# Kernel optimization log

Measured on AMD Instinct MI355X. Metric: run time of the kernel, lower is better.

The kernel has to match this reference:

```python
import jax, jax.numpy as jnp
import numpy as np

N, CX, CS, H = 2048, 768, 384, 16
D = CX // H  # 48


def _ln(t, eps=1e-5):
    mu = jnp.mean(t, axis=-1, keepdims=True)
    var = jnp.mean(jnp.square(t - mu), axis=-1, keepdims=True)
    return (t - mu) * jax.lax.rsqrt(var + eps)


def setup_inputs() -> dict:
    key = jax.random.key(0)
    ks = jax.random.split(key, 16)
    s = 0.02
    return {
        "x": jax.random.normal(ks[0], (N, CX), jnp.float32),
        "mask": jax.random.randint(ks[1], (N,), 0, 2, jnp.int32),
        "pair_logits": jax.random.normal(ks[2], (H, N, N), jnp.float32),
        "single_cond": jax.random.normal(ks[3], (N, CS), jnp.float32),
        # AdaptiveLayerNorm params (single_cond LN has weight, no bias)
        "ln_sc_w": jnp.ones((CS,), jnp.float32),
        "sc_scale_w": s * jax.random.normal(ks[4], (CS, CX), jnp.float32),
        "sc_scale_b": jnp.zeros((CX,), jnp.float32),
        "sc_bias_w": s * jax.random.normal(ks[5], (CS, CX), jnp.float32),
        # q/k/v/gating projections (stored as (in, out); y = x @ W)
        "q_w": s * jax.random.normal(ks[6], (CX, CX), jnp.float32),
        "q_b": jnp.zeros((CX,), jnp.float32),
        "k_w": s * jax.random.normal(ks[7], (CX, CX), jnp.float32),
        "v_w": s * jax.random.normal(ks[8], (CX, CX), jnp.float32),
        "gate_w": s * jax.random.normal(ks[9], (CX, CX), jnp.float32),
        # AdaLNZero params
        "out_w": s * jax.random.normal(ks[10], (CX, CX), jnp.float32),
        "azc_w": s * jax.random.normal(ks[11], (CS, CX), jnp.float32),
        "azc_b": jnp.zeros((CX,), jnp.float32),
    }


def reference(x, mask, pair_logits, single_cond, ln_sc_w, sc_scale_w, sc_scale_b,
              sc_bias_w, q_w, q_b, k_w, v_w, gate_w, out_w, azc_w, azc_b):
    # AdaptiveLayerNorm (use_single_cond=True)
    xn = _ln(x)                              # (N, CX), no affine
    sc = _ln(single_cond) * ln_sc_w          # (N, CS), weight only
    xa = jax.nn.sigmoid(sc @ sc_scale_w + sc_scale_b) * xn + sc @ sc_bias_w

    # QKV projections, split into heads: (N, H, D)
    q = (xa @ q_w + q_b).reshape(N, H, D)
    k = (xa @ k_w).reshape(N, H, D)
    v = (xa @ v_w).reshape(N, H, D)

    # Attention with per-head additive pair bias and key mask
    logits = jnp.einsum("qhd,khd->hqk", q * (D ** -0.5), k) + pair_logits
    logits = jnp.where(mask.astype(bool)[None, None, :], logits, -1e9)
    w = jax.nn.softmax(logits, axis=-1)      # (H, N, N)
    wa = jnp.einsum("hqk,khd->qhd", w, v).reshape(N, CX)

    # Gating, then AdaLNZero output
    wa = wa * jax.nn.sigmoid(xa @ gate_w)
    out = (wa @ out_w) * jax.nn.sigmoid(sc @ azc_w + azc_b)
    return out
```

## Files before the change

kernel.cpp:

```cpp
#include <hip/hip_runtime.h>
#include <math.h>

#define NN 2048
#define CXX 768
#define CSS 384
#define HH 16
#define DHH 48

typedef short bf16x8 __attribute__((ext_vector_type(8)));
typedef float f32x4 __attribute__((ext_vector_type(4)));

#define MFMA16(a,b,c) __builtin_amdgcn_mfma_f32_16x16x32_bf16(a,b,c,0,0,0)

__device__ __forceinline__ unsigned short f2bf(float f){
  unsigned u = __float_as_uint(f);
  u += 0x7FFFu + ((u >> 16) & 1u);
  return (unsigned short)(u >> 16);
}
__device__ __forceinline__ float bf2f(unsigned short u){
  return __uint_as_float(((unsigned)u) << 16);
}
__device__ __forceinline__ void async_copy16(const void* g, void* l){
  __builtin_amdgcn_global_load_lds((const __attribute__((address_space(1))) void*)g,
                                   (__attribute__((address_space(3))) void*)l, 16, 0, 0);
}

__device__ inline float waveReduceSum(float v){
  #pragma unroll
  for(int o=32;o>0;o>>=1) v += __shfl_xor(v,o);
  return v;
}

__global__ __launch_bounds__(256) void transpose_bf16(const float* __restrict__ W,
    unsigned short* __restrict__ Wt, int K, int Ncols){
  __shared__ unsigned short t[32][33];
  int n0 = blockIdx.x*32, k0 = blockIdx.y*32;
  int c = threadIdx.x & 31, r = threadIdx.x >> 5;
  #pragma unroll
  for(int i=0;i<32;i+=8){
    float v = W[(size_t)(k0 + r + i)*Ncols + n0 + c];
    t[c][r+i] = f2bf(v);
  }
  __syncthreads();
  #pragma unroll
  for(int i=0;i<32;i+=8){
    Wt[(size_t)(n0 + r + i)*K + k0 + c] = t[r+i][c];
  }
}

__global__ __launch_bounds__(256) void ln_x_kernel(const float* __restrict__ x,
                                                   float* __restrict__ xn){
  int row = blockIdx.x;
  int t = threadIdx.x;
  const float* xr = x + (size_t)row*CXX;
  float v0 = xr[t], v1 = xr[t+256], v2 = xr[t+512];
  float s = v0+v1+v2;
  __shared__ float red[4], red2[4];
  s = waveReduceSum(s);
  if((t&63)==0) red[t>>6] = s;
  __syncthreads();
  float mu = (red[0]+red[1]+red[2]+red[3]) * (1.0f/CXX);
  float d0=v0-mu, d1=v1-mu, d2=v2-mu;
  float q = d0*d0+d1*d1+d2*d2;
  q = waveReduceSum(q);
  if((t&63)==0) red2[t>>6] = q;
  __syncthreads();
  float var = (red2[0]+red2[1]+red2[2]+red2[3]) * (1.0f/CXX);
  float r = rsqrtf(var + 1e-5f);
  float* o = xn + (size_t)row*CXX;
  o[t] = d0*r; o[t+256] = d1*r; o[t+512] = d2*r;
}

__global__ __launch_bounds__(128) void ln_sc_kernel(const float* __restrict__ scin,
                                                    const float* __restrict__ w,
                                                    unsigned short* __restrict__ sc){
  int row = blockIdx.x;
  int t = threadIdx.x;
  const float* xr = scin + (size_t)row*CSS;
  float v0 = xr[t], v1 = xr[t+128], v2 = xr[t+256];
  float s = v0+v1+v2;
  __shared__ float red[2], red2[2];
  s = waveReduceSum(s);
  if((t&63)==0) red[t>>6] = s;
  __syncthreads();
  float mu = (red[0]+red[1]) * (1.0f/CSS);
  float d0=v0-mu, d1=v1-mu, d2=v2-mu;
  float q = d0*d0+d1*d1+d2*d2;
  q = waveReduceSum(q);
  if((t&63)==0) red2[t>>6] = q;
  __syncthreads();
  float var = (red2[0]+red2[1]) * (1.0f/CSS);
  float r = rsqrtf(var + 1e-5f);
  unsigned short* o = sc + (size_t)row*CSS;
  o[t]     = f2bf(d0*r*w[t]);
  o[t+128] = f2bf(d1*r*w[t+128]);
  o[t+256] = f2bf(d2*r*w[t+256]);
}

template<int K, int NC, int MODE>
__global__ __launch_bounds__(256) void gemm_mfma(const unsigned short* __restrict__ A,
    const unsigned short* __restrict__ Bt, const float* __restrict__ bias,
    const float* __restrict__ mul, void* __restrict__ Cp){
  __shared__ unsigned short As[128*32];
  __shared__ unsigned short Bs[128*32];
  const int tid = threadIdx.x;
  const int w = tid>>6, lane = tid&63;
  const int ln15 = lane&15, hi = lane>>4;
  const int wm = w&1, wn = w>>1;
  const int m0 = blockIdx.y*128, n0 = blockIdx.x*128;
  const int lrow = lane>>2, lk = (lane&3)*8;

  f32x4 z = {0.f,0.f,0.f,0.f};
  f32x4 acc[4][4];
  #pragma unroll
  for(int i=0;i<4;i++)
    #pragma unroll
    for(int j=0;j<4;j++) acc[i][j] = z;

  for(int k0=0;k0<K;k0+=32){
    const unsigned short* ga = A + (size_t)(m0 + w*32 + lrow)*K + k0 + lk;
    const unsigned short* gb = Bt + (size_t)(n0 + w*32 + lrow)*K + k0 + lk;
    async_copy16(ga,          &As[w*1024]);
    async_copy16(ga + 16*K,   &As[w*1024 + 512]);
    async_copy16(gb,          &Bs[w*1024]);
    async_copy16(gb + 16*K,   &Bs[w*1024 + 512]);
    __syncthreads();
    bf16x8 af[4], bfr[4];
    #pragma unroll
    for(int i=0;i<4;i++) af[i]  = *(const bf16x8*)&As[(wm*64 + i*16 + ln15)*32 + hi*8];
    #pragma unroll
    for(int j=0;j<4;j++) bfr[j] = *(const bf16x8*)&Bs[(wn*64 + j*16 + ln15)*32 + hi*8];
    #pragma unroll
    for(int i=0;i<4;i++)
      #pragma unroll
      for(int j=0;j<4;j++)
        acc[i][j] = MFMA16(af[i], bfr[j], acc[i][j]);
    __syncthreads();
  }

  #pragma unroll
  for(int i=0;i<4;i++){
    #pragma unroll
    for(int j=0;j<4;j++){
      #pragma unroll
      for(int r=0;r<4;r++){
        int gm = m0 + wm*64 + i*16 + hi*4 + r;
        int gn = n0 + wn*64 + j*16 + ln15;
        float v = acc[i][j][r];
        if constexpr (MODE == 0){
          if(gn < 768) v += bias[gn];
          if(gn >= 2304) v = 1.0f/(1.0f + __expf(-v));
          ((unsigned short*)Cp)[(size_t)gm*NC + gn] = f2bf(v);
        } else if constexpr (MODE == 1){
          v = 1.0f/(1.0f + __expf(-(v + bias[gn])));
          ((float*)Cp)[(size_t)gm*NC + gn] = v;
        } else {
          ((float*)Cp)[(size_t)gm*NC + gn] = v * mul[(size_t)gm*NC + gn];
        }
      }
    }
  }
}

__global__ __launch_bounds__(256) void adaln_mfma(const unsigned short* __restrict__ A,
    const unsigned short* __restrict__ B1, const unsigned short* __restrict__ B2,
    const float* __restrict__ bs, const float* __restrict__ xn,
    unsigned short* __restrict__ xa){
  __shared__ unsigned short As[128*32];
  __shared__ unsigned short Bs1[128*32];
  __shared__ unsigned short Bs2[128*32];
  const int tid = threadIdx.x;
  const int w = tid>>6, lane = tid&63;
  const int ln15 = lane&15, hi = lane>>4;
  const int wm = w&1, wn = w>>1;
  const int m0 = blockIdx.y*128, n0 = blockIdx.x*128;
  const int lrow = lane>>2, lk = (lane&3)*8;

  f32x4 z = {0.f,0.f,0.f,0.f};
  f32x4 acc1[4][4], acc2[4][4];
  #pragma unroll
  for(int i=0;i<4;i++)
    #pragma unroll
    for(int j=0;j<4;j++){ acc1[i][j] = z; acc2[i][j] = z; }

  for(int k0=0;k0<CSS;k0+=32){
    const unsigned short* ga  = A  + (size_t)(m0 + w*32 + lrow)*CSS + k0 + lk;
    const unsigned short* gb1 = B1 + (size_t)(n0 + w*32 + lrow)*CSS + k0 + lk;
    const unsigned short* gb2 = B2 + (size_t)(n0 + w*32 + lrow)*CSS + k0 + lk;
    async_copy16(ga,            &As[w*1024]);
    async_copy16(ga  + 16*CSS,  &As[w*1024 + 512]);
    async_copy16(gb1,           &Bs1[w*1024]);
    async_copy16(gb1 + 16*CSS,  &Bs1[w*1024 + 512]);
    async_copy16(gb2,           &Bs2[w*1024]);
    async_copy16(gb2 + 16*CSS,  &Bs2[w*1024 + 512]);
    __syncthreads();
    bf16x8 af[4], b1f[4], b2f[4];
    #pragma unroll
    for(int i=0;i<4;i++) af[i]  = *(const bf16x8*)&As[(wm*64 + i*16 + ln15)*32 + hi*8];
    #pragma unroll
    for(int j=0;j<4;j++){
      b1f[j] = *(const bf16x8*)&Bs1[(wn*64 + j*16 + ln15)*32 + hi*8];
      b2f[j] = *(const bf16x8*)&Bs2[(wn*64 + j*16 + ln15)*32 + hi*8];
    }
    #pragma unroll
    for(int i=0;i<4;i++)
      #pragma unroll
      for(int j=0;j<4;j++){
        acc1[i][j] = MFMA16(af[i], b1f[j], acc1[i][j]);
        acc2[i][j] = MFMA16(af[i], b2f[j], acc2[i][j]);
      }
    __syncthreads();
  }

  #pragma unroll
  for(int i=0;i<4;i++)
    #pragma unroll
    for(int j=0;j<4;j++)
      #pragma unroll
      for(int r=0;r<4;r++){
        int gm = m0 + wm*64 + i*16 + hi*4 + r;
        int gn = n0 + wn*64 + j*16 + ln15;
        float g = 1.0f/(1.0f + __expf(-(acc1[i][j][r] + bs[gn])));
        float v = g * xn[(size_t)gm*CXX + gn] + acc2[i][j][r];
        xa[(size_t)gm*CXX + gn] = f2bf(v);
      }
}

__global__ __launch_bounds__(256) void attn_mfma(const unsigned short* __restrict__ qkvg,
    const float* __restrict__ pair, const int* __restrict__ mask,
    unsigned short* __restrict__ wag){
  const int h = blockIdx.y;
  const int q0 = blockIdx.x*64;
  const int tid = threadIdx.x;
  const int w = tid>>6, lane = tid&63;
  const int ln15 = lane&15, hi = lane>>4;

  __shared__ unsigned short Qs[64*72];
  __shared__ unsigned short Ks[64*72];
  __shared__ unsigned short VsT[48*72];
  __shared__ unsigned short Ps[4][16*72];

  for(int idx=tid; idx<64*16; idx+=256){
    int row = idx>>4, d = 48 + (idx&15);
    Qs[row*72 + d] = 0;
    Ks[row*72 + d] = 0;
  }
  for(int idx=tid; idx<64*12; idx+=256){
    int qr = idx&63, d0 = (idx>>6)*4;
    ushort4 v = *(const ushort4*)&qkvg[(size_t)(q0+qr)*3072 + h*DHH + d0];
    *(ushort4*)&Qs[qr*72 + d0] = v;
  }
  __syncthreads();

  bf16x8 aq0 = *(const bf16x8*)&Qs[(w*16+ln15)*72 + hi*8];
  bf16x8 aq1 = *(const bf16x8*)&Qs[(w*16+ln15)*72 + 32 + hi*8];

  f32x4 z = {0.f,0.f,0.f,0.f};
  f32x4 oacc[3] = {z,z,z};
  float mold[4] = {-1e30f,-1e30f,-1e30f,-1e30f};
  float l[4] = {0.f,0.f,0.f,0.f};
  const float scale = 0.14433756729740643f;
  const int qrb = w*16 + hi*4;

  for(int kt=0; kt<NN/64; ++kt){
    int k0 = kt*64;
    __syncthreads();
    for(int idx=tid; idx<64*12; idx+=256){
      int key = idx&63, d0 = (idx>>6)*4;
      ushort4 kv = *(const ushort4*)&qkvg[(size_t)(k0+key)*3072 +  768 + h*DHH + d0];
      *(ushort4*)&Ks[key*72 + d0] = kv;
      ushort4 vv = *(const ushort4*)&qkvg[(size_t)(k0+key)*3072 + 1536 + h*DHH + d0];
      VsT[(d0+0)*72 + key] = vv.x;
      VsT[(d0+1)*72 + key] = vv.y;
      VsT[(d0+2)*72 + key] = vv.z;
      VsT[(d0+3)*72 + key] = vv.w;
    }
    __syncthreads();

    int msk[4];
    float pr[4][4];
    #pragma unroll
    for(int jt=0;jt<4;jt++) msk[jt] = mask[k0 + jt*16 + ln15];
    const float* pb = pair + ((size_t)h*NN + (size_t)(q0+qrb))*NN + k0 + ln15;
    #pragma unroll
    for(int r=0;r<4;r++)
      #pragma unroll
      for(int jt=0;jt<4;jt++)
        pr[jt][r] = pb[(size_t)r*NN + jt*16];

    f32x4 sreg[4];
    #pragma unroll
    for(int jt=0;jt<4;jt++){
      bf16x8 bk0 = *(const bf16x8*)&Ks[(jt*16+ln15)*72 + hi*8];
      bf16x8 bk1 = *(const bf16x8*)&Ks[(jt*16+ln15)*72 + 32 + hi*8];
      f32x4 s = z;
      s = MFMA16(aq0, bk0, s);
      s = MFMA16(aq1, bk1, s);
      sreg[jt] = s;
    }

    float sv[4][4];
    #pragma unroll
    for(int jt=0;jt<4;jt++)
      #pragma unroll
      for(int r=0;r<4;r++)
        sv[jt][r] = msk[jt] ? sreg[jt][r]*scale + pr[jt][r] : -1e9f;

    float mr[4], al[4], rs[4];
    #pragma unroll
    for(int r=0;r<4;r++)
      mr[r] = fmaxf(fmaxf(sv[0][r],sv[1][r]), fmaxf(sv[2][r],sv[3][r]));
    #pragma unroll
    for(int o=1;o<16;o<<=1)
      #pragma unroll
      for(int r=0;r<4;r++) mr[r] = fmaxf(mr[r], __shfl_xor(mr[r],o));
    #pragma unroll
    for(int r=0;r<4;r++){
      float mn = fmaxf(mold[r], mr[r]);
      al[r] = __expf(mold[r] - mn);
      mold[r] = mn;
    }
    float pv[4][4];
    #pragma unroll
    for(int jt=0;jt<4;jt++)
      #pragma unroll
      for(int r=0;r<4;r++)
        pv[jt][r] = __expf(sv[jt][r] - mold[r]);
    #pragma unroll
    for(int r=0;r<4;r++) rs[r] = pv[0][r]+pv[1][r]+pv[2][r]+pv[3][r];
    #pragma unroll
    for(int o=1;o<16;o<<=1)
      #pragma unroll
      for(int r=0;r<4;r++) rs[r] += __shfl_xor(rs[r],o);
    #pragma unroll
    for(int r=0;r<4;r++) l[r] = l[r]*al[r] + rs[r];

    #pragma unroll
    for(int jt=0;jt<4;jt++)
      #pragma unroll
      for(int r=0;r<4;r++)
        Ps[w][(hi*4+r)*72 + jt*16 + ln15] = f2bf(pv[jt][r]);
    __asm__ volatile("s_waitcnt lgkmcnt(0)" ::: "memory");

    #pragma unroll
    for(int dt=0;dt<3;dt++)
      #pragma unroll
      for(int r=0;r<4;r++) oacc[dt][r] *= al[r];

    bf16x8 ap0 = *(const bf16x8*)&Ps[w][ln15*72 + hi*8];
    bf16x8 ap1 = *(const bf16x8*)&Ps[w][ln15*72 + 32 + hi*8];
    #pragma unroll
    for(int dt=0;dt<3;dt++){
      bf16x8 bv0 = *(const bf16x8*)&VsT[(dt*16+ln15)*72 + hi*8];
      bf16x8 bv1 = *(const bf16x8*)&VsT[(dt*16+ln15)*72 + 32 + hi*8];
      oacc[dt] = MFMA16(ap0, bv0, oacc[dt]);
      oacc[dt] = MFMA16(ap1, bv1, oacc[dt]);
    }
  }

  #pragma unroll
  for(int r=0;r<4;r++){
    float linv = 1.0f / l[r];
    int qrow = q0 + qrb + r;
    #pragma unroll
    for(int dt=0;dt<3;dt++){
      int col = h*DHH + dt*16 + ln15;
      float g = bf2f(qkvg[(size_t)qrow*3072 + 2304 + col]);
      float o = oacc[dt][r] * linv * g;
      wag[(size_t)qrow*CXX + col] = f2bf(o);
    }
  }
}

extern "C" void kernel_launch(void* const* d_in, const int* in_sizes, int n_in,
                              void* d_out, int out_size, void* d_ws, size_t ws_size,
                              hipStream_t stream) {
  const float* x           = (const float*)d_in[0];
  const int*   mask        = (const int*)  d_in[1];
  const float* pair        = (const float*)d_in[2];
  const float* single_cond = (const float*)d_in[3];
  const float* ln_sc_w     = (const float*)d_in[4];
  const float* sc_scale_w  = (const float*)d_in[5];
  const float* sc_scale_b  = (const float*)d_in[6];
  const float* sc_bias_w   = (const float*)d_in[7];
  const float* q_w         = (const float*)d_in[8];
  const float* q_b         = (const float*)d_in[9];
  const float* k_w         = (const float*)d_in[10];
  const float* v_w         = (const float*)d_in[11];
  const float* gate_w      = (const float*)d_in[12];
  const float* out_w       = (const float*)d_in[13];
  const float* azc_w       = (const float*)d_in[14];
  const float* azc_b       = (const float*)d_in[15];
  float* out = (float*)d_out;

  unsigned short* p = (unsigned short*)d_ws;
  unsigned short* Wt_scale = p;  p += 768*384;
  unsigned short* Wt_bias  = p;  p += 768*384;
  unsigned short* Wt_azc   = p;  p += 768*384;
  unsigned short* Wt_out   = p;  p += 768*768;
  unsigned short* Wt_qkvg  = p;  p += 3072*768;
  unsigned short* scb      = p;  p += 2048*384;
  unsigned short* xa       = p;  p += 2048*768;
  unsigned short* qkvg     = p;  p += (size_t)2048*3072;
  unsigned short* wag      = p;  p += 2048*768;
  float* fp = (float*)p;
  float* xn  = fp; fp += (size_t)2048*768;
  float* azc = fp;

  dim3 t24_12(24,12), t24_24(24,24);
  transpose_bf16<<<t24_12, 256, 0, stream>>>(sc_scale_w, Wt_scale, 384, 768);
  transpose_bf16<<<t24_12, 256, 0, stream>>>(sc_bias_w,  Wt_bias,  384, 768);
  transpose_bf16<<<t24_12, 256, 0, stream>>>(azc_w,      Wt_azc,   384, 768);
  transpose_bf16<<<t24_24, 256, 0, stream>>>(q_w,    Wt_qkvg + 0*589824, 768, 768);
  transpose_bf16<<<t24_24, 256, 0, stream>>>(k_w,    Wt_qkvg + 1*589824, 768, 768);
  transpose_bf16<<<t24_24, 256, 0, stream>>>(v_w,    Wt_qkvg + 2*589824, 768, 768);
  transpose_bf16<<<t24_24, 256, 0, stream>>>(gate_w, Wt_qkvg + 3*589824, 768, 768);
  transpose_bf16<<<t24_24, 256, 0, stream>>>(out_w,  Wt_out, 768, 768);

  ln_x_kernel <<<NN, 256, 0, stream>>>(x, xn);
  ln_sc_kernel<<<NN, 128, 0, stream>>>(single_cond, ln_sc_w, scb);

  adaln_mfma<<<dim3(6,16), 256, 0, stream>>>(scb, Wt_scale, Wt_bias, sc_scale_b, xn, xa);
  gemm_mfma<768,3072,0><<<dim3(24,16), 256, 0, stream>>>(xa, Wt_qkvg, q_b, nullptr, qkvg);
  gemm_mfma<384,768,1><<<dim3(6,16), 256, 0, stream>>>(scb, Wt_azc, azc_b, nullptr, azc);

  attn_mfma<<<dim3(32,16), 256, 0, stream>>>(qkvg, pair, mask, wag);

  gemm_mfma<768,768,2><<<dim3(6,16), 256, 0, stream>>>(wag, Wt_out, nullptr, azc, out);
}
```

Measured before the change: 541.1 us.

## Fuse small kernels, retile adaLN/out GEMMs, and prefetch attention K/V/pair tiles

Merges the eight weight transposes into one launch and the two layernorms into one kernel. Folds the azc GEMM into the adaLN kernel and shrinks the adaLN and output GEMMs to 64x64 tiles so more blocks fill the CUs. In attention, register-prefetches the next K/V tile, mask and pair-logit values while the current tile computes, hiding global latency at the cost of extra registers. Launch overhead and underoccupancy on the small GEMMs are the main targets.

```diff
diff --git a/kernel.cpp b/kernel.cpp
--- a/kernel.cpp
+++ b/kernel.cpp
@@ -31,14 +31,32 @@
   return v;
 }
 
-__global__ __launch_bounds__(256) void transpose_bf16(const float* __restrict__ W,
-    unsigned short* __restrict__ Wt, int K, int Ncols){
+__global__ __launch_bounds__(256) void transpose_all(
+    const float* __restrict__ s0, const float* __restrict__ s1, const float* __restrict__ s2,
+    const float* __restrict__ s3, const float* __restrict__ s4, const float* __restrict__ s5,
+    const float* __restrict__ s6, const float* __restrict__ s7,
+    unsigned short* __restrict__ d_scale, unsigned short* __restrict__ d_bias,
+    unsigned short* __restrict__ d_azc, unsigned short* __restrict__ d_qkvg,
+    unsigned short* __restrict__ d_out){
+  int z = blockIdx.z;
+  const float* W; unsigned short* Wt; int K;
+  switch(z){
+    case 0: W=s0; Wt=d_scale; K=384; break;
+    case 1: W=s1; Wt=d_bias;  K=384; break;
+    case 2: W=s2; Wt=d_azc;   K=384; break;
+    case 3: W=s3; Wt=d_qkvg + 0*589824; K=768; break;
+    case 4: W=s4; Wt=d_qkvg + 1*589824; K=768; break;
+    case 5: W=s5; Wt=d_qkvg + 2*589824; K=768; break;
+    case 6: W=s6; Wt=d_qkvg + 3*589824; K=768; break;
+    default: W=s7; Wt=d_out; K=768; break;
+  }
+  int n0 = blockIdx.x*32, k0 = blockIdx.y*32;
+  if(k0 >= K) return;
   __shared__ unsigned short t[32][33];
-  int n0 = blockIdx.x*32, k0 = blockIdx.y*32;
   int c = threadIdx.x & 31, r = threadIdx.x >> 5;
   #pragma unroll
   for(int i=0;i<32;i+=8){
-    float v = W[(size_t)(k0 + r + i)*Ncols + n0 + c];
+    float v = W[(size_t)(k0 + r + i)*CXX + n0 + c];
     t[c][r+i] = f2bf(v);
   }
   __syncthreads();
@@ -48,59 +66,47 @@
   }
 }
 
-__global__ __launch_bounds__(256) void ln_x_kernel(const float* __restrict__ x,
-                                                   float* __restrict__ xn){
+__global__ __launch_bounds__(384) void ln_fused(const float* __restrict__ x,
+    const float* __restrict__ scin, const float* __restrict__ w,
+    float* __restrict__ xn, unsigned short* __restrict__ scb){
   int row = blockIdx.x;
   int t = threadIdx.x;
-  const float* xr = x + (size_t)row*CXX;
-  float v0 = xr[t], v1 = xr[t+256], v2 = xr[t+512];
-  float s = v0+v1+v2;
-  __shared__ float red[4], red2[4];
-  s = waveReduceSum(s);
-  if((t&63)==0) red[t>>6] = s;
-  __syncthreads();
-  float mu = (red[0]+red[1]+red[2]+red[3]) * (1.0f/CXX);
-  float d0=v0-mu, d1=v1-mu, d2=v2-mu;
-  float q = d0*d0+d1*d1+d2*d2;
-  q = waveReduceSum(q);
-  if((t&63)==0) red2[t>>6] = q;
-  __syncthreads();
-  float var = (red2[0]+red2[1]+red2[2]+red2[3]) * (1.0f/CXX);
+  int wid = t>>6, lane = t&63;
+  __shared__ float red[6];
+  float a0 = x[(size_t)row*CXX + t];
+  float a1 = x[(size_t)row*CXX + 384 + t];
+  float s = waveReduceSum(a0+a1);
+  if(lane==0) red[wid]=s;
+  __syncthreads();
+  float mu = (red[0]+red[1]+red[2]+red[3]+red[4]+red[5]) * (1.0f/CXX);
+  float d0=a0-mu, d1=a1-mu;
+  float q = waveReduceSum(d0*d0+d1*d1);
+  __syncthreads();
+  if(lane==0) red[wid]=q;
+  __syncthreads();
+  float var = (red[0]+red[1]+red[2]+red[3]+red[4]+red[5]) * (1.0f/CXX);
   float r = rsqrtf(var + 1e-5f);
-  float* o = xn + (size_t)row*CXX;
-  o[t] = d0*r; o[t+256] = d1*r; o[t+512] = d2*r;
-}
-
-__global__ __launch_bounds__(128) void ln_sc_kernel(const float* __restrict__ scin,
-                                                    const float* __restrict__ w,
-                                                    unsigned short* __restrict__ sc){
-  int row = blockIdx.x;
-  int t = threadIdx.x;
-  const float* xr = scin + (size_t)row*CSS;
-  float v0 = xr[t], v1 = xr[t+128], v2 = xr[t+256];
-  float s = v0+v1+v2;
-  __shared__ float red[2], red2[2];
-  s = waveReduceSum(s);
-  if((t&63)==0) red[t>>6] = s;
-  __syncthreads();
-  float mu = (red[0]+red[1]) * (1.0f/CSS);
-  float d0=v0-mu, d1=v1-mu, d2=v2-mu;
-  float q = d0*d0+d1*d1+d2*d2;
-  q = waveReduceSum(q);
-  if((t&63)==0) red2[t>>6] = q;
-  __syncthreads();
-  float var = (red2[0]+red2[1]) * (1.0f/CSS);
-  float r = rsqrtf(var + 1e-5f);
-  unsigned short* o = sc + (size_t)row*CSS;
-  o[t]     = f2bf(d0*r*w[t]);
-  o[t+128] = f2bf(d1*r*w[t+128]);
-  o[t+256] = f2bf(d2*r*w[t+256]);
-}
-
-template<int K, int NC, int MODE>
-__global__ __launch_bounds__(256) void gemm_mfma(const unsigned short* __restrict__ A,
+  xn[(size_t)row*CXX + t] = d0*r;
+  xn[(size_t)row*CXX + 384 + t] = d1*r;
+  float b = scin[(size_t)row*CSS + t];
+  float s2 = waveReduceSum(b);
+  __syncthreads();
+  if(lane==0) red[wid]=s2;
+  __syncthreads();
+  float mu2 = (red[0]+red[1]+red[2]+red[3]+red[4]+red[5]) * (1.0f/CSS);
+  float d2 = b - mu2;
+  float q2 = waveReduceSum(d2*d2);
+  __syncthreads();
+  if(lane==0) red[wid]=q2;
+  __syncthreads();
+  float var2 = (red[0]+red[1]+red[2]+red[3]+red[4]+red[5]) * (1.0f/CSS);
+  float r2 = rsqrtf(var2 + 1e-5f);
+  scb[(size_t)row*CSS + t] = f2bf(d2*r2*w[t]);
+}
+
+__global__ __launch_bounds__(256) void gemm_qkvg(const unsigned short* __restrict__ A,
     const unsigned short* __restrict__ Bt, const float* __restrict__ bias,
-    const float* __restrict__ mul, void* __restrict__ Cp){
+    unsigned short* __restrict__ C){
   __shared__ unsigned short As[128*32];
   __shared__ unsigned short Bs[128*32];
   const int tid = threadIdx.x;
@@ -109,6 +115,7 @@
   const int wm = w&1, wn = w>>1;
   const int m0 = blockIdx.y*128, n0 = blockIdx.x*128;
   const int lrow = lane>>2, lk = (lane&3)*8;
+  const int K = 768, NC = 3072;
 
   f32x4 z = {0.f,0.f,0.f,0.f};
   f32x4 acc[4][4];
@@ -139,90 +146,131 @@
   }
 
   #pragma unroll
-  for(int i=0;i<4;i++){
-    #pragma unroll
-    for(int j=0;j<4;j++){
+  for(int i=0;i<4;i++)
+    #pragma unroll
+    for(int j=0;j<4;j++)
       #pragma unroll
       for(int r=0;r<4;r++){
         int gm = m0 + wm*64 + i*16 + hi*4 + r;
         int gn = n0 + wn*64 + j*16 + ln15;
         float v = acc[i][j][r];
-        if constexpr (MODE == 0){
-          if(gn < 768) v += bias[gn];
-          if(gn >= 2304) v = 1.0f/(1.0f + __expf(-v));
-          ((unsigned short*)Cp)[(size_t)gm*NC + gn] = f2bf(v);
-        } else if constexpr (MODE == 1){
-          v = 1.0f/(1.0f + __expf(-(v + bias[gn])));
-          ((float*)Cp)[(size_t)gm*NC + gn] = v;
-        } else {
-          ((float*)Cp)[(size_t)gm*NC + gn] = v * mul[(size_t)gm*NC + gn];
-        }
+        if(gn < 768) v += bias[gn];
+        if(gn >= 2304) v = 1.0f/(1.0f + __expf(-v));
+        C[(size_t)gm*NC + gn] = f2bf(v);
       }
-    }
-  }
-}
-
-__global__ __launch_bounds__(256) void adaln_mfma(const unsigned short* __restrict__ A,
+}
+
+__global__ __launch_bounds__(256) void adaln3(const unsigned short* __restrict__ A,
     const unsigned short* __restrict__ B1, const unsigned short* __restrict__ B2,
-    const float* __restrict__ bs, const float* __restrict__ xn,
-    unsigned short* __restrict__ xa){
-  __shared__ unsigned short As[128*32];
-  __shared__ unsigned short Bs1[128*32];
-  __shared__ unsigned short Bs2[128*32];
+    const unsigned short* __restrict__ B3, const float* __restrict__ bs,
+    const float* __restrict__ zb, const float* __restrict__ xn,
+    unsigned short* __restrict__ xa, float* __restrict__ azc){
+  __shared__ unsigned short As[64*32];
+  __shared__ unsigned short Bs1[64*32];
+  __shared__ unsigned short Bs2[64*32];
+  __shared__ unsigned short Bs3[64*32];
   const int tid = threadIdx.x;
   const int w = tid>>6, lane = tid&63;
   const int ln15 = lane&15, hi = lane>>4;
   const int wm = w&1, wn = w>>1;
-  const int m0 = blockIdx.y*128, n0 = blockIdx.x*128;
-  const int lrow = lane>>2, lk = (lane&3)*8;
+  const int m0 = blockIdx.y*64, n0 = blockIdx.x*64;
+  const int lrow = tid>>2, lk = (tid&3)*8;
+  const int K = CSS;
 
   f32x4 z = {0.f,0.f,0.f,0.f};
-  f32x4 acc1[4][4], acc2[4][4];
-  #pragma unroll
-  for(int i=0;i<4;i++)
-    #pragma unroll
-    for(int j=0;j<4;j++){ acc1[i][j] = z; acc2[i][j] = z; }
-
-  for(int k0=0;k0<CSS;k0+=32){
-    const unsigned short* ga  = A  + (size_t)(m0 + w*32 + lrow)*CSS + k0 + lk;
-    const unsigned short* gb1 = B1 + (size_t)(n0 + w*32 + lrow)*CSS + k0 + lk;
-    const unsigned short* gb2 = B2 + (size_t)(n0 + w*32 + lrow)*CSS + k0 + lk;
-    async_copy16(ga,            &As[w*1024]);
-    async_copy16(ga  + 16*CSS,  &As[w*1024 + 512]);
-    async_copy16(gb1,           &Bs1[w*1024]);
-    async_copy16(gb1 + 16*CSS,  &Bs1[w*1024 + 512]);
-    async_copy16(gb2,           &Bs2[w*1024]);
-    async_copy16(gb2 + 16*CSS,  &Bs2[w*1024 + 512]);
-    __syncthreads();
-    bf16x8 af[4], b1f[4], b2f[4];
-    #pragma unroll
-    for(int i=0;i<4;i++) af[i]  = *(const bf16x8*)&As[(wm*64 + i*16 + ln15)*32 + hi*8];
-    #pragma unroll
-    for(int j=0;j<4;j++){
-      b1f[j] = *(const bf16x8*)&Bs1[(wn*64 + j*16 + ln15)*32 + hi*8];
-      b2f[j] = *(const bf16x8*)&Bs2[(wn*64 + j*16 + ln15)*32 + hi*8];
-    }
-    #pragma unroll
-    for(int i=0;i<4;i++)
-      #pragma unroll
-      for(int j=0;j<4;j++){
+  f32x4 acc1[2][2], acc2[2][2], acc3[2][2];
+  #pragma unroll
+  for(int i=0;i<2;i++)
+    #pragma unroll
+    for(int j=0;j<2;j++){ acc1[i][j]=z; acc2[i][j]=z; acc3[i][j]=z; }
+
+  for(int k0=0;k0<K;k0+=32){
+    async_copy16(A  + (size_t)(m0+lrow)*K + k0 + lk, &As [w*512]);
+    async_copy16(B1 + (size_t)(n0+lrow)*K + k0 + lk, &Bs1[w*512]);
+    async_copy16(B2 + (size_t)(n0+lrow)*K + k0 + lk, &Bs2[w*512]);
+    async_copy16(B3 + (size_t)(n0+lrow)*K + k0 + lk, &Bs3[w*512]);
+    __syncthreads();
+    bf16x8 af[2], b1f[2], b2f[2], b3f[2];
+    #pragma unroll
+    for(int i=0;i<2;i++) af[i]  = *(const bf16x8*)&As[(wm*32 + i*16 + ln15)*32 + hi*8];
+    #pragma unroll
+    for(int j=0;j<2;j++){
+      b1f[j] = *(const bf16x8*)&Bs1[(wn*32 + j*16 + ln15)*32 + hi*8];
+      b2f[j] = *(const bf16x8*)&Bs2[(wn*32 + j*16 + ln15)*32 + hi*8];
+      b3f[j] = *(const bf16x8*)&Bs3[(wn*32 + j*16 + ln15)*32 + hi*8];
+    }
+    #pragma unroll
+    for(int i=0;i<2;i++)
+      #pragma unroll
+      for(int j=0;j<2;j++){
         acc1[i][j] = MFMA16(af[i], b1f[j], acc1[i][j]);
         acc2[i][j] = MFMA16(af[i], b2f[j], acc2[i][j]);
+        acc3[i][j] = MFMA16(af[i], b3f[j], acc3[i][j]);
       }
     __syncthreads();
   }
 
   #pragma unroll
-  for(int i=0;i<4;i++)
-    #pragma unroll
-    for(int j=0;j<4;j++)
+  for(int i=0;i<2;i++)
+    #pragma unroll
+    for(int j=0;j<2;j++)
       #pragma unroll
       for(int r=0;r<4;r++){
-        int gm = m0 + wm*64 + i*16 + hi*4 + r;
-        int gn = n0 + wn*64 + j*16 + ln15;
+        int gm = m0 + wm*32 + i*16 + hi*4 + r;
+        int gn = n0 + wn*32 + j*16 + ln15;
         float g = 1.0f/(1.0f + __expf(-(acc1[i][j][r] + bs[gn])));
         float v = g * xn[(size_t)gm*CXX + gn] + acc2[i][j][r];
         xa[(size_t)gm*CXX + gn] = f2bf(v);
+        azc[(size_t)gm*CXX + gn] = 1.0f/(1.0f + __expf(-(acc3[i][j][r] + zb[gn])));
+      }
+}
+
+__global__ __launch_bounds__(256) void gemm_out(const unsigned short* __restrict__ A,
+    const unsigned short* __restrict__ Bt, const float* __restrict__ mul,
+    float* __restrict__ C){
+  __shared__ unsigned short As[64*32];
+  __shared__ unsigned short Bs[64*32];
+  const int tid = threadIdx.x;
+  const int w = tid>>6, lane = tid&63;
+  const int ln15 = lane&15, hi = lane>>4;
+  const int wm = w&1, wn = w>>1;
+  const int m0 = blockIdx.y*64, n0 = blockIdx.x*64;
+  const int lrow = tid>>2, lk = (tid&3)*8;
+  const int K = 768;
+
+  f32x4 z = {0.f,0.f,0.f,0.f};
+  f32x4 acc[2][2];
+  #pragma unroll
+  for(int i=0;i<2;i++)
+    #pragma unroll
+    for(int j=0;j<2;j++) acc[i][j]=z;
+
+  for(int k0=0;k0<K;k0+=32){
+    async_copy16(A  + (size_t)(m0+lrow)*K + k0 + lk, &As[w*512]);
+    async_copy16(Bt + (size_t)(n0+lrow)*K + k0 + lk, &Bs[w*512]);
+    __syncthreads();
+    bf16x8 af[2], bfr[2];
+    #pragma unroll
+    for(int i=0;i<2;i++) af[i]  = *(const bf16x8*)&As[(wm*32 + i*16 + ln15)*32 + hi*8];
+    #pragma unroll
+    for(int j=0;j<2;j++) bfr[j] = *(const bf16x8*)&Bs[(wn*32 + j*16 + ln15)*32 + hi*8];
+    #pragma unroll
+    for(int i=0;i<2;i++)
+      #pragma unroll
+      for(int j=0;j<2;j++)
+        acc[i][j] = MFMA16(af[i], bfr[j], acc[i][j]);
+    __syncthreads();
+  }
+
+  #pragma unroll
+  for(int i=0;i<2;i++)
+    #pragma unroll
+    for(int j=0;j<2;j++)
+      #pragma unroll
+      for(int r=0;r<4;r++){
+        int gm = m0 + wm*32 + i*16 + hi*4 + r;
+        int gn = n0 + wn*32 + j*16 + ln15;
+        C[(size_t)gm*CXX + gn] = acc[i][j][r] * mul[(size_t)gm*CXX + gn];
       }
 }
 
@@ -262,14 +310,36 @@
   const float scale = 0.14433756729740643f;
   const int qrb = w*16 + hi*4;
 
+  ushort4 kreg[3], vreg[3];
+  int mreg[4];
+  float preg[4][4];
+  {
+    #pragma unroll
+    for(int it=0;it<3;it++){
+      int idx = tid + it*256;
+      int key = idx&63, d0 = (idx>>6)*4;
+      kreg[it] = *(const ushort4*)&qkvg[(size_t)key*3072 +  768 + h*DHH + d0];
+      vreg[it] = *(const ushort4*)&qkvg[(size_t)key*3072 + 1536 + h*DHH + d0];
+    }
+    #pragma unroll
+    for(int jt=0;jt<4;jt++) mreg[jt] = mask[jt*16 + ln15];
+    const float* pb = pair + ((size_t)h*NN + (size_t)(q0+qrb))*NN + ln15;
+    #pragma unroll
+    for(int r=0;r<4;r++)
+      #pragma unroll
+      for(int jt=0;jt<4;jt++)
+        preg[jt][r] = pb[(size_t)r*NN + jt*16];
+  }
+
   for(int kt=0; kt<NN/64; ++kt){
-    int k0 = kt*64;
-    __syncthreads();
-    for(int idx=tid; idx<64*12; idx+=256){
+    __syncthreads();
+    #pragma unroll
+    for(int it=0;it<3;it++){
+      int idx = tid + it*256;
       int key = idx&63, d0 = (idx>>6)*4;
-      ushort4 kv = *(const ushort4*)&qkvg[(size_t)(k0+key)*3072 +  768 + h*DHH + d0];
+      ushort4 kv = kreg[it];
       *(ushort4*)&Ks[key*72 + d0] = kv;
-      ushort4 vv = *(const ushort4*)&qkvg[(size_t)(k0+key)*3072 + 1536 + h*DHH + d0];
+      ushort4 vv = vreg[it];
       VsT[(d0+0)*72 + key] = vv.x;
       VsT[(d0+1)*72 + key] = vv.y;
       VsT[(d0+2)*72 + key] = vv.z;
@@ -277,16 +347,31 @@
     }
     __syncthreads();
 
-    int msk[4];
-    float pr[4][4];
-    #pragma unroll
-    for(int jt=0;jt<4;jt++) msk[jt] = mask[k0 + jt*16 + ln15];
-    const float* pb = pair + ((size_t)h*NN + (size_t)(q0+qrb))*NN + k0 + ln15;
-    #pragma unroll
-    for(int r=0;r<4;r++)
-      #pragma unroll
-      for(int jt=0;jt<4;jt++)
-        pr[jt][r] = pb[(size_t)r*NN + jt*16];
+    float pc[4][4]; int mc[4];
+    #pragma unroll
+    for(int jt=0;jt<4;jt++){
+      mc[jt] = mreg[jt];
+      #pragma unroll
+      for(int r=0;r<4;r++) pc[jt][r] = preg[jt][r];
+    }
+    {
+      int k0n = (kt < NN/64 - 1) ? (kt+1)*64 : 0;
+      #pragma unroll
+      for(int it=0;it<3;it++){
+        int idx = tid + it*256;
+        int key = idx&63, d0 = (idx>>6)*4;
+        kreg[it] = *(const ushort4*)&qkvg[(size_t)(k0n+key)*3072 +  768 + h*DHH + d0];
+        vreg[it] = *(const ushort4*)&qkvg[(size_t)(k0n+key)*3072 + 1536 + h*DHH + d0];
+      }
+      #pragma unroll
+      for(int jt=0;jt<4;jt++) mreg[jt] = mask[k0n + jt*16 + ln15];
+      const float* pb = pair + ((size_t)h*NN + (size_t)(q0+qrb))*NN + k0n + ln15;
+      #pragma unroll
+      for(int r=0;r<4;r++)
+        #pragma unroll
+        for(int jt=0;jt<4;jt++)
+          preg[jt][r] = pb[(size_t)r*NN + jt*16];
+    }
 
     f32x4 sreg[4];
     #pragma unroll
@@ -304,7 +389,7 @@
     for(int jt=0;jt<4;jt++)
       #pragma unroll
       for(int r=0;r<4;r++)
-        sv[jt][r] = msk[jt] ? sreg[jt][r]*scale + pr[jt][r] : -1e9f;
+        sv[jt][r] = mc[jt] ? sreg[jt][r]*scale + pc[jt][r] : -1e9f;
 
     float mr[4], al[4], rs[4];
     #pragma unroll
@@ -398,7 +483,7 @@
   unsigned short* Wt_bias  = p;  p += 768*384;
   unsigned short* Wt_azc   = p;  p += 768*384;
   unsigned short* Wt_out   = p;  p += 768*768;
-  unsigned short* Wt_qkvg  = p;  p += 3072*768;
+  unsigned short* Wt_qkvg  = p;  p += (size_t)3072*768;
   unsigned short* scb      = p;  p += 2048*384;
   unsigned short* xa       = p;  p += 2048*768;
   unsigned short* qkvg     = p;  p += (size_t)2048*3072;
@@ -407,24 +492,18 @@
   float* xn  = fp; fp += (size_t)2048*768;
   float* azc = fp;
 
-  dim3 t24_12(24,12), t24_24(24,24);
-  transpose_bf16<<<t24_12, 256, 0, stream>>>(sc_scale_w, Wt_scale, 384, 768);
-  transpose_bf16<<<t24_12, 256, 0, stream>>>(sc_bias_w,  Wt_bias,  384, 768);
-  transpose_bf16<<<t24_12, 256, 0, stream>>>(azc_w,      Wt_azc,   384, 768);
-  transpose_bf16<<<t24_24, 256, 0, stream>>>(q_w,    Wt_qkvg + 0*589824, 768, 768);
-  transpose_bf16<<<t24_24, 256, 0, stream>>>(k_w,    Wt_qkvg + 1*589824, 768, 768);
-  transpose_bf16<<<t24_24, 256, 0, stream>>>(v_w,    Wt_qkvg + 2*589824, 768, 768);
-  transpose_bf16<<<t24_24, 256, 0, stream>>>(gate_w, Wt_qkvg + 3*589824, 768, 768);
-  transpose_bf16<<<t24_24, 256, 0, stream>>>(out_w,  Wt_out, 768, 768);
-
-  ln_x_kernel <<<NN, 256, 0, stream>>>(x, xn);
-  ln_sc_kernel<<<NN, 128, 0, stream>>>(single_cond, ln_sc_w, scb);
-
-  adaln_mfma<<<dim3(6,16), 256, 0, stream>>>(scb, Wt_scale, Wt_bias, sc_scale_b, xn, xa);
-  gemm_mfma<768,3072,0><<<dim3(24,16), 256, 0, stream>>>(xa, Wt_qkvg, q_b, nullptr, qkvg);
-  gemm_mfma<384,768,1><<<dim3(6,16), 256, 0, stream>>>(scb, Wt_azc, azc_b, nullptr, azc);
+  transpose_all<<<dim3(24,24,8), 256, 0, stream>>>(
+      sc_scale_w, sc_bias_w, azc_w, q_w, k_w, v_w, gate_w, out_w,
+      Wt_scale, Wt_bias, Wt_azc, Wt_qkvg, Wt_out);
+
+  ln_fused<<<NN, 384, 0, stream>>>(x, single_cond, ln_sc_w, xn, scb);
+
+  adaln3<<<dim3(12,32), 256, 0, stream>>>(scb, Wt_scale, Wt_bias, Wt_azc,
+                                          sc_scale_b, azc_b, xn, xa, azc);
+
+  gemm_qkvg<<<dim3(24,16), 256, 0, stream>>>(xa, Wt_qkvg, q_b, qkvg);
 
   attn_mfma<<<dim3(32,16), 256, 0, stream>>>(qkvg, pair, mask, wag);
 
-  gemm_mfma<768,768,2><<<dim3(6,16), 256, 0, stream>>>(wag, Wt_out, nullptr, azc, out);
-}
+  gemm_out<<<dim3(12,32), 256, 0, stream>>>(wag, Wt_out, azc, out);
+}
```

After: 506.5 us. 1.07x faster.
